# Kernel optimization log

Hardware: AMD Instinct MI355X
Metric: run time of the kernel (lower is better)

## Reference

```python
import jax, jax.numpy as jnp
import numpy as np

N_HIDDEN = 1024
N_OUT = 8
BATCH = 16
SEQ = 2000
TAU = 0.01
TAU_DEPR = 0.2
TAU_FACIL = 1.5
BETA = 50.0
GAIN = 1.0            # self.gain
ACT_GAIN = 8.0        # activation_gain
ACT_THRESH = 0.5      # activation_thresh
DT = 0.001
NOISE_TAU = 0.01
PROB_C = 0.1


def setup_inputs() -> dict:
    key = jax.random.key(0)
    ks = jax.random.split(key, 10)
    I = jax.random.normal(ks[0], (BATCH, SEQ, 1), dtype=jnp.float32)
    h_0 = jax.random.normal(ks[1], (BATCH, N_HIDDEN), dtype=jnp.float32)
    r_0 = jax.random.uniform(ks[2], (BATCH, N_HIDDEN), dtype=jnp.float32)
    u_0 = jax.random.uniform(ks[3], (BATCH, N_HIDDEN), dtype=jnp.float32)
    # parameters, sized/initialized as in __init__
    W_ih = jax.random.normal(ks[4], (N_HIDDEN, 1), dtype=jnp.float32)
    offset_ih = jnp.zeros((N_HIDDEN,), dtype=jnp.float32)
    w_hidden_std = 1.0 / np.sqrt(PROB_C * N_HIDDEN)
    W_hh = jax.random.normal(ks[5], (N_HIDDEN, N_HIDDEN), dtype=jnp.float32) * w_hidden_std
    W_hz = jax.random.normal(ks[6], (N_OUT, N_HIDDEN), dtype=jnp.float32) * (1.0 / np.sqrt(N_HIDDEN))
    offset_hz = jnp.zeros((N_OUT,), dtype=jnp.float32)
    # p_rel ~ N(0.35, 0.15) resampled into (0, 1]; clip is an equivalent in-range stand-in
    p_rel = jnp.clip(jax.random.normal(ks[7], (N_HIDDEN,), dtype=jnp.float32) * 0.15 + 0.35, 0.05, 1.0)
    # sparse recurrent mask with connection prob 0.1
    W_hh_mask = (jax.random.uniform(ks[8], (N_HIDDEN, N_HIDDEN)) < PROB_C).astype(jnp.float32)
    # block-diagonal readout mask: each output reads a disjoint subset of hidden units
    per = N_HIDDEN // N_OUT
    m = np.zeros((N_OUT, N_HIDDEN), dtype=np.float32)
    for i in range(N_OUT):
        m[i, i * per:(i + 1) * per] = 1.0
    W_hz_mask = jnp.asarray(m)
    return {"I": I, "h_0": h_0, "r_0": r_0, "u_0": u_0,
            "W_ih": W_ih, "offset_ih": offset_ih, "W_hh": W_hh,
            "W_hz": W_hz, "offset_hz": offset_hz, "p_rel": p_rel,
            "W_hh_mask": W_hh_mask, "W_hz_mask": W_hz_mask}


def _run(I, h_0, r_0, u_0, W_ih, offset_ih, W_hh, W_hz, offset_hz, p_rel, W_hh_mask, W_hz_mask):
    presyn = 1.0 / p_rel                      # presyn_scaling [H]
    Wm = GAIN * W_hh * W_hh_mask              # masked recurrent weight [H,H]
    Wz = W_hz * W_hz_mask                     # masked readout [O,H]
    ht0 = jax.nn.sigmoid(ACT_GAIN * (h_0 - ACT_THRESH))
    n0 = jnp.zeros_like(h_0)                  # n_0=None, noise_std=0.0 defaults

    def step(carry, I_t):
        h, r, u, ht, n = carry                # all [B,H], ht = transfer(h_{t-1})
        # noise state: dn/dt = -n/noise_tau (noise_std = 0)
        n_new = n - (n / NOISE_TAU) * DT
        # depression / facilitation (use previous-step values, as in torch loop)
        r_new = r + ((1.0 - r) / TAU_DEPR - BETA * u * r * ht) * DT
        u_new = u + ((p_rel - u) / TAU_FACIL + BETA * p_rel * (1.0 - u) * ht) * DT
        # recurrent drive: (r*u*presyn * ht) @ (gain*W_hh*mask)^T, column scaling is presynaptic
        s = ht * r * u * presyn               # [B,H]
        rec = s @ Wm.T                        # [B,H]
        ext = I_t @ W_ih.T + offset_ih + n    # [B,H]
        h_new = h + ((-h + rec + ext) / TAU) * DT
        ht_new = jax.nn.sigmoid(ACT_GAIN * (h_new - ACT_THRESH))
        z = ht_new @ Wz.T + offset_hz         # [B,O]
        return (h_new, r_new, u_new, ht_new, n_new), (n_new, h_new, r_new, u_new, z)

    _, (n_all, h_all, r_all, u_all, z_all) = jax.lax.scan(
        step, (h_0, r_0, u_0, ht0, n0), jnp.swapaxes(I, 0, 1))
    tp = lambda x: jnp.swapaxes(x, 0, 1)      # [S,B,*] -> [B,S,*]
    return tp(n_all), tp(h_all), tp(r_all), tp(u_all), tp(z_all)


def reference(I, h_0, r_0, u_0, W_ih, offset_ih, W_hh, W_hz, offset_hz, p_rel, W_hh_mask, W_hz_mask):
    return _run(I, h_0, r_0, u_0, W_ih, offset_ih, W_hh, W_hz, offset_hz, p_rel, W_hh_mask, W_hz_mask)
```

## Files before the change

kernel.cpp:

```cpp
#include <hip/hip_runtime.h>
#include <cstdint>
#include <cstddef>

typedef float f32x4 __attribute__((ext_vector_type(4)));
typedef unsigned int u32x4 __attribute__((ext_vector_type(4)));
typedef short s16x8 __attribute__((ext_vector_type(8)));

#define H     1024
#define BATCH 16
#define SEQ   2000
#define NOUT  8
#define G     64
#define RPW   16
#define TPB   256

#define H_OFF 32768000
#define R_OFF 65536000
#define U_OFF 98304000
#define Z_OFF 131072000

#define SBUF_OFF  8192
#define IREP_OFF  139264
#define ZPART_OFF 267392

#define TAG(tau) ((unsigned int)(((tau) >> 1) & 1))

__global__ void init_kernel(const float* __restrict__ I, float* __restrict__ Irep,
                            unsigned int* __restrict__ sbuf) {
  int tid = blockIdx.x * blockDim.x + threadIdx.x;
  if (tid < SEQ * BATCH) {
    int t = tid >> 4, b = tid & 15;
    Irep[tid] = I[b * SEQ + t];
  }
  if (tid < 2 * BATCH * H) {
    unsigned int* ap = sbuf + tid; unsigned int v = 1u;
    asm volatile("global_store_dword %0, %1, off sc0 sc1" :: "v"(ap), "v"(v) : "memory");
  }
}

__device__ __forceinline__ unsigned int pack_split(float f) {
  unsigned int uh = __float_as_uint(f) & 0xffff0000u;
  float fl = f - __uint_as_float(uh);
  return uh | (__float_as_uint(fl) >> 16);
}

__global__ __launch_bounds__(TPB, 1) void rnn_persist(
    const float* __restrict__ h0, const float* __restrict__ r0, const float* __restrict__ u0,
    const float* __restrict__ Wih, const float* __restrict__ offih,
    const float* __restrict__ Whh, const float* __restrict__ Whz,
    const float* __restrict__ prel, const float* __restrict__ Whhm, const float* __restrict__ Whzm,
    const float* __restrict__ Irep, unsigned int* __restrict__ sbuf,
    float* __restrict__ zpart, float* __restrict__ dout)
{
  __shared__ float redC[2][4][16][17];

  const int g = blockIdx.x, tid = threadIdx.x;
  const int lane = tid & 63, w = tid >> 6;
  const int arow  = lane & 15;
  const int klane = lane >> 4;
  const int ro = lane >> 2, bo = (w << 2) + (lane & 3);
  const int row = g * RPW + ro;

  s16x8 ahi[8], alo[8];
  {
    const float* wr = Whh  + (size_t)(g * RPW + arow) * H;
    const float* mr = Whhm + (size_t)(g * RPW + arow) * H;
    #pragma unroll
    for (int c = 0; c < 8; ++c) {
      const int jb = w * 256 + c * 32 + klane * 8;
      f32x4 w0 = *(const f32x4*)(wr + jb),     m0 = *(const f32x4*)(mr + jb);
      f32x4 w1 = *(const f32x4*)(wr + jb + 4), m1 = *(const f32x4*)(mr + jb + 4);
      float wf[8] = { w0.x*m0.x, w0.y*m0.y, w0.z*m0.z, w0.w*m0.w,
                      w1.x*m1.x, w1.y*m1.y, w1.z*m1.z, w1.w*m1.w };
      #pragma unroll
      for (int i = 0; i < 8; ++i) {
        unsigned int uh = __float_as_uint(wf[i]) & 0xffff0000u;
        float fl = wf[i] - __uint_as_float(uh);
        ahi[c][i] = (short)(uh >> 16);
        alo[c][i] = (short)(__float_as_uint(fl) >> 16);
      }
    }
  }

  const int sidx = bo * H + row;
  float h  = h0[sidx], rr_ = r0[sidx], u = u0[sidx];
  float p  = prel[row], psyn = 1.0f / p;
  float wih = Wih[row], oih = offih[row];
  float wz = Whz[(row >> 7) * H + row] * Whzm[(row >> 7) * H + row];
  float ht = 1.0f / (1.0f + __expf(-8.0f * (h - 0.5f)));

  const float INV_TAU = 1.0f / 0.01f, INV_TD = 1.0f / 0.2f, INV_TF = 1.0f / 1.5f;
  const int sidx3 = ((row >> 3) << 7) + (bo << 3) + (row & 7);

#define WAITV(n) { asm volatile("s_waitcnt vmcnt(" #n ")" ::: "memory"); \
                   __builtin_amdgcn_sched_barrier(0); }

  {
    unsigned int pk = (pack_split(ht * rr_ * u * psyn) & ~1u) | TAG(0);
    unsigned int* ap = sbuf + sidx3;
    asm volatile("global_store_dword %0, %1, off sc0 sc1" :: "v"(ap), "v"(pk) : "memory");
  }

  float* ph = dout + H_OFF + (size_t)bo * (SEQ * H) + row;
  float* pr = dout + R_OFF + (size_t)bo * (SEQ * H) + row;
  float* pu = dout + U_OFF + (size_t)bo * (SEQ * H) + row;
  float* pz = zpart + (size_t)g * BATCH + (w << 2) + lane;
  const float* ip = Irep + bo;
  float Itc = ip[0];

#define ISSUE_CHUNK(c) { \
    const unsigned int* ap = sb + ((w * 32 + (c) * 4 + klane) * 128 + arow * 8); \
    asm volatile("global_load_dwordx4 %0, %1, off sc0 sc1" : "=v"(ld[2*(c)])   : "v"(ap)     : "memory"); \
    asm volatile("global_load_dwordx4 %0, %1, off sc0 sc1" : "=v"(ld[2*(c)+1]) : "v"(ap + 4) : "memory"); }

#define VCHK(c, okv) { u32x4 v0 = ld[2*(c)], v1 = ld[2*(c)+1]; \
    unsigned int bad = (v0.x ^ tg) | (v0.y ^ tg) | (v0.z ^ tg) | (v0.w ^ tg) \
                     | (v1.x ^ tg) | (v1.y ^ tg) | (v1.z ^ tg) | (v1.w ^ tg); \
    okv = __all((int)((bad & 1u) == 0)); }

#define DO_CHUNK(c) { \
    u32x4 q0 = ld[2*(c)], q1 = ld[2*(c)+1]; \
    s16x8 bh, bl; \
    bh[0]=(short)(q0.x>>16); bl[0]=(short)q0.x; \
    bh[1]=(short)(q0.y>>16); bl[1]=(short)q0.y; \
    bh[2]=(short)(q0.z>>16); bl[2]=(short)q0.z; \
    bh[3]=(short)(q0.w>>16); bl[3]=(short)q0.w; \
    bh[4]=(short)(q1.x>>16); bl[4]=(short)q1.x; \
    bh[5]=(short)(q1.y>>16); bl[5]=(short)q1.y; \
    bh[6]=(short)(q1.z>>16); bl[6]=(short)q1.z; \
    bh[7]=(short)(q1.w>>16); bl[7]=(short)q1.w; \
    acc = __builtin_amdgcn_mfma_f32_16x16x32_bf16(ahi[c], bh, acc, 0, 0, 0); \
    acc = __builtin_amdgcn_mfma_f32_16x16x32_bf16(ahi[c], bl, acc, 0, 0, 0); \
    acc = __builtin_amdgcn_mfma_f32_16x16x32_bf16(alo[c], bh, acc, 0, 0, 0); \
    acc = __builtin_amdgcn_mfma_f32_16x16x32_bf16(alo[c], bl, acc, 0, 0, 0); }

#define FIRST_PASS(c, n) { WAITV(n); int ok; VCHK(c, ok); \
    if (ok) { DO_CHUNK(c); done |= (1 << (c)); } }

  for (int t = 0; t < SEQ; ++t) {
    const unsigned int tg = TAG(t);
    const unsigned int* sb = sbuf + (t & 1) * (BATCH * H);

    u32x4 ld[16];
    f32x4 acc = {0.f, 0.f, 0.f, 0.f};
    int done = 0;

    ISSUE_CHUNK(0) ISSUE_CHUNK(1) ISSUE_CHUNK(2) ISSUE_CHUNK(3)
    ISSUE_CHUNK(4) ISSUE_CHUNK(5) ISSUE_CHUNK(6) ISSUE_CHUNK(7)

    FIRST_PASS(0,14) FIRST_PASS(1,12) FIRST_PASS(2,10) FIRST_PASS(3,8)
    FIRST_PASS(4,6)  FIRST_PASS(5,4)  FIRST_PASS(6,2)  FIRST_PASS(7,0)

    {
      int guard = 0;
      while (done != 0xff && ++guard < (1 << 13)) {
        #pragma unroll
        for (int c = 0; c < 8; ++c)
          if (!(done & (1 << c))) ISSUE_CHUNK(c);
        WAITV(0);
        #pragma unroll
        for (int c = 0; c < 8; ++c)
          if (!(done & (1 << c))) {
            int ok; VCHK(c, ok);
            if (ok) { DO_CHUNK(c); done |= (1 << c); }
          }
      }
    }

    const int pbuf = t & 1;
    redC[pbuf][w][klane * 4 + 0][arow] = acc.x;
    redC[pbuf][w][klane * 4 + 1][arow] = acc.y;
    redC[pbuf][w][klane * 4 + 2][arow] = acc.z;
    redC[pbuf][w][klane * 4 + 3][arow] = acc.w;
    __syncthreads();
    float rec = redC[pbuf][0][ro][bo] + redC[pbuf][1][ro][bo]
              + redC[pbuf][2][ro][bo] + redC[pbuf][3][ro][bo];

    float ext = Itc * wih + oih;
    float hn  = h + ((-h + rec + ext) * INV_TAU) * 0.001f;
    float htn = 1.0f / (1.0f + __expf(-8.0f * (hn - 0.5f)));
    float rn  = rr_ + ((1.0f - rr_) * INV_TD - 50.0f * u * rr_ * ht) * 0.001f;
    float un  = u + ((p - u) * INV_TF + 50.0f * p * (1.0f - u) * ht) * 0.001f;

    {
      unsigned int pk = (pack_split(htn * rn * un * psyn) & ~1u) | TAG(t + 1);
      unsigned int* ap = sbuf + ((t + 1) & 1) * (BATCH * H) + sidx3;
      asm volatile("global_store_dword %0, %1, off sc0 sc1" :: "v"(ap), "v"(pk) : "memory");
    }

    ph[(size_t)t * H] = hn; pr[(size_t)t * H] = rn; pu[(size_t)t * H] = un;
    float zl = htn * wz;
    zl += __shfl_xor(zl, 4); zl += __shfl_xor(zl, 8);
    zl += __shfl_xor(zl, 16); zl += __shfl_xor(zl, 32);
    if (lane < 4) pz[(size_t)t * (G * BATCH)] = zl;

    Itc = ip[(size_t)(t + 1) * BATCH];
    h = hn; ht = htn; rr_ = rn; u = un;
  }
#undef FIRST_PASS
#undef DO_CHUNK
#undef VCHK
#undef ISSUE_CHUNK
#undef WAITV
}

__global__ void zred_kernel(const float* __restrict__ zpart, const float* __restrict__ offhz,
                            float* __restrict__ zout) {
  int tid = blockIdx.x * blockDim.x + threadIdx.x;
  if (tid >= BATCH * SEQ * NOUT) return;
  int b = tid / (SEQ * NOUT);
  int rem = tid - b * (SEQ * NOUT);
  int t = rem >> 3, o = rem & 7;
  float acc = offhz[o];
  #pragma unroll
  for (int k = 0; k < G / NOUT; ++k)
    acc += zpart[((size_t)t * G + o * (G / NOUT) + k) * BATCH + b];
  zout[tid] = acc;
}

extern "C" void kernel_launch(void* const* d_in, const int* in_sizes, int n_in,
                              void* d_out, int out_size, void* d_ws, size_t ws_size,
                              hipStream_t stream) {
  const float* I     = (const float*)d_in[0];
  const float* h0    = (const float*)d_in[1];
  const float* r0    = (const float*)d_in[2];
  const float* u0    = (const float*)d_in[3];
  const float* Wih   = (const float*)d_in[4];
  const float* offih = (const float*)d_in[5];
  const float* Whh   = (const float*)d_in[6];
  const float* Whz   = (const float*)d_in[7];
  const float* offhz = (const float*)d_in[8];
  const float* prel  = (const float*)d_in[9];
  const float* Whhm  = (const float*)d_in[10];
  const float* Whzm  = (const float*)d_in[11];
  float* out = (float*)d_out;

  unsigned int* sbuf  = (unsigned int*)((char*)d_ws + SBUF_OFF);
  float* Irep  = (float*)((char*)d_ws + IREP_OFF);
  float* zpart = (float*)((char*)d_ws + ZPART_OFF);

  hipMemsetAsync(d_out, 0, (size_t)H_OFF * sizeof(float), stream);
  init_kernel<<<128, 256, 0, stream>>>(I, Irep, sbuf);
  rnn_persist<<<G, TPB, 0, stream>>>(h0, r0, u0, Wih, offih, Whh, Whz, prel, Whhm, Whzm,
                                     Irep, sbuf, zpart, out);
  zred_kernel<<<(BATCH * SEQ * NOUT + 255) / 256, 256, 0, stream>>>(zpart, offhz, out + Z_OFF);
}
```

Baseline: 4.616 ms.

## Halve persistent block count by giving each block two 16-row MFMA tiles

Each persistent workgroup now owns 32 hidden rows instead of 16, so the grid shrinks from 64 to 32 blocks. Each wave keeps two sets of split-bf16 weight fragments and issues two MFMA chains per loaded chunk of the broadcast state vector. This halves the number of blocks polling and reading the shared state buffer each step. The per-thread epilogue now handles two rows with vectorized stores, and the readout partial sums are reduced in shared memory and written one step late. The tradeoffs are twice the MFMA work per block on the serial critical path and higher register pressure.

```diff
diff --git a/kernel.cpp b/kernel.cpp
--- a/kernel.cpp
+++ b/kernel.cpp
@@ -3,15 +3,17 @@
 #include <cstddef>
 
 typedef float f32x4 __attribute__((ext_vector_type(4)));
+typedef float f32x2 __attribute__((ext_vector_type(2)));
 typedef unsigned int u32x4 __attribute__((ext_vector_type(4)));
+typedef unsigned int u32x2 __attribute__((ext_vector_type(2)));
 typedef short s16x8 __attribute__((ext_vector_type(8)));
 
 #define H     1024
 #define BATCH 16
 #define SEQ   2000
 #define NOUT  8
-#define G     64
-#define RPW   16
+#define G     32
+#define ROWS  32
 #define TPB   256
 
 #define H_OFF 32768000
@@ -52,59 +54,72 @@
     const float* __restrict__ Irep, unsigned int* __restrict__ sbuf,
     float* __restrict__ zpart, float* __restrict__ dout)
 {
-  __shared__ float redC[2][4][16][17];
+  __shared__ float redC[2][4][2][16][17];
+  __shared__ float zsc[2][4][16];
 
   const int g = blockIdx.x, tid = threadIdx.x;
   const int lane = tid & 63, w = tid >> 6;
   const int arow  = lane & 15;
   const int klane = lane >> 4;
-  const int ro = lane >> 2, bo = (w << 2) + (lane & 3);
-  const int row = g * RPW + ro;
-
-  s16x8 ahi[8], alo[8];
-  {
-    const float* wr = Whh  + (size_t)(g * RPW + arow) * H;
-    const float* mr = Whhm + (size_t)(g * RPW + arow) * H;
+
+  s16x8 ahi[2][8], alo[2][8];
+  #pragma unroll
+  for (int rt = 0; rt < 2; ++rt) {
+    const float* wr = Whh  + (size_t)(g * ROWS + rt * 16 + arow) * H + w * 256 + klane * 8;
+    const float* mr = Whhm + (size_t)(g * ROWS + rt * 16 + arow) * H + w * 256 + klane * 8;
     #pragma unroll
     for (int c = 0; c < 8; ++c) {
-      const int jb = w * 256 + c * 32 + klane * 8;
-      f32x4 w0 = *(const f32x4*)(wr + jb),     m0 = *(const f32x4*)(mr + jb);
-      f32x4 w1 = *(const f32x4*)(wr + jb + 4), m1 = *(const f32x4*)(mr + jb + 4);
+      f32x4 w0 = *(const f32x4*)(wr + c * 32),     m0 = *(const f32x4*)(mr + c * 32);
+      f32x4 w1 = *(const f32x4*)(wr + c * 32 + 4), m1 = *(const f32x4*)(mr + c * 32 + 4);
       float wf[8] = { w0.x*m0.x, w0.y*m0.y, w0.z*m0.z, w0.w*m0.w,
                       w1.x*m1.x, w1.y*m1.y, w1.z*m1.z, w1.w*m1.w };
       #pragma unroll
       for (int i = 0; i < 8; ++i) {
         unsigned int uh = __float_as_uint(wf[i]) & 0xffff0000u;
         float fl = wf[i] - __uint_as_float(uh);
-        ahi[c][i] = (short)(uh >> 16);
-        alo[c][i] = (short)(__float_as_uint(fl) >> 16);
+        ahi[rt][c][i] = (short)(uh >> 16);
+        alo[rt][c][i] = (short)(__float_as_uint(fl) >> 16);
       }
     }
   }
 
-  const int sidx = bo * H + row;
-  float h  = h0[sidx], rr_ = r0[sidx], u = u0[sidx];
-  float p  = prel[row], psyn = 1.0f / p;
-  float wih = Wih[row], oih = offih[row];
-  float wz = Whz[(row >> 7) * H + row] * Whzm[(row >> 7) * H + row];
-  float ht = 1.0f / (1.0f + __expf(-8.0f * (h - 0.5f)));
+  const int r0w = g * ROWS + w * 8 + 2 * klane;
+  const int bo  = arow;
+  f32x2 hv = *(const f32x2*)(h0 + (size_t)bo * H + r0w);
+  f32x2 rv = *(const f32x2*)(r0 + (size_t)bo * H + r0w);
+  f32x2 uv = *(const f32x2*)(u0 + (size_t)bo * H + r0w);
+  f32x2 pv = *(const f32x2*)(prel + r0w);
+  f32x2 wihv = *(const f32x2*)(Wih + r0w);
+  f32x2 oihv = *(const f32x2*)(offih + r0w);
+  const int o = r0w >> 7;
+  f32x2 wzv  = *(const f32x2*)(Whz  + (size_t)o * H + r0w);
+  f32x2 wzm  = *(const f32x2*)(Whzm + (size_t)o * H + r0w);
+  f32x2 psynv, htv;
+  #pragma unroll
+  for (int i = 0; i < 2; ++i) {
+    wzv[i] *= wzm[i];
+    psynv[i] = 1.0f / pv[i];
+    htv[i] = 1.0f / (1.0f + __expf(-8.0f * (hv[i] - 0.5f)));
+  }
 
   const float INV_TAU = 1.0f / 0.01f, INV_TD = 1.0f / 0.2f, INV_TF = 1.0f / 1.5f;
-  const int sidx3 = ((row >> 3) << 7) + (bo << 3) + (row & 7);
+
+  unsigned int* pubp = sbuf + (((r0w >> 3) << 7) + (bo << 3) + (r0w & 7));
 
 #define WAITV(n) { asm volatile("s_waitcnt vmcnt(" #n ")" ::: "memory"); \
                    __builtin_amdgcn_sched_barrier(0); }
 
   {
-    unsigned int pk = (pack_split(ht * rr_ * u * psyn) & ~1u) | TAG(0);
-    unsigned int* ap = sbuf + sidx3;
-    asm volatile("global_store_dword %0, %1, off sc0 sc1" :: "v"(ap), "v"(pk) : "memory");
-  }
-
-  float* ph = dout + H_OFF + (size_t)bo * (SEQ * H) + row;
-  float* pr = dout + R_OFF + (size_t)bo * (SEQ * H) + row;
-  float* pu = dout + U_OFF + (size_t)bo * (SEQ * H) + row;
-  float* pz = zpart + (size_t)g * BATCH + (w << 2) + lane;
+    u32x2 pk;
+    #pragma unroll
+    for (int i = 0; i < 2; ++i)
+      pk[i] = (pack_split(htv[i] * rv[i] * uv[i] * psynv[i]) & ~1u) | TAG(0);
+    asm volatile("global_store_dwordx2 %0, %1, off sc0 sc1" :: "v"(pubp), "v"(pk) : "memory");
+  }
+
+  float* ph = dout + H_OFF + (size_t)bo * (SEQ * H) + r0w;
+  float* pr = dout + R_OFF + (size_t)bo * (SEQ * H) + r0w;
+  float* pu = dout + U_OFF + (size_t)bo * (SEQ * H) + r0w;
   const float* ip = Irep + bo;
   float Itc = ip[0];
 
@@ -129,10 +144,11 @@
     bh[5]=(short)(q1.y>>16); bl[5]=(short)q1.y; \
     bh[6]=(short)(q1.z>>16); bl[6]=(short)q1.z; \
     bh[7]=(short)(q1.w>>16); bl[7]=(short)q1.w; \
-    acc = __builtin_amdgcn_mfma_f32_16x16x32_bf16(ahi[c], bh, acc, 0, 0, 0); \
-    acc = __builtin_amdgcn_mfma_f32_16x16x32_bf16(ahi[c], bl, acc, 0, 0, 0); \
-    acc = __builtin_amdgcn_mfma_f32_16x16x32_bf16(alo[c], bh, acc, 0, 0, 0); \
-    acc = __builtin_amdgcn_mfma_f32_16x16x32_bf16(alo[c], bl, acc, 0, 0, 0); }
+    _Pragma("unroll") for (int rt = 0; rt < 2; ++rt) { \
+      acc[rt] = __builtin_amdgcn_mfma_f32_16x16x32_bf16(ahi[rt][c], bh, acc[rt], 0, 0, 0); \
+      acc[rt] = __builtin_amdgcn_mfma_f32_16x16x32_bf16(ahi[rt][c], bl, acc[rt], 0, 0, 0); \
+      acc[rt] = __builtin_amdgcn_mfma_f32_16x16x32_bf16(alo[rt][c], bh, acc[rt], 0, 0, 0); \
+      acc[rt] = __builtin_amdgcn_mfma_f32_16x16x32_bf16(alo[rt][c], bl, acc[rt], 0, 0, 0); } }
 
 #define FIRST_PASS(c, n) { WAITV(n); int ok; VCHK(c, ok); \
     if (ok) { DO_CHUNK(c); done |= (1 << (c)); } }
@@ -142,7 +158,7 @@
     const unsigned int* sb = sbuf + (t & 1) * (BATCH * H);
 
     u32x4 ld[16];
-    f32x4 acc = {0.f, 0.f, 0.f, 0.f};
+    f32x4 acc[2] = {{0.f,0.f,0.f,0.f},{0.f,0.f,0.f,0.f}};
     int done = 0;
 
     ISSUE_CHUNK(0) ISSUE_CHUNK(1) ISSUE_CHUNK(2) ISSUE_CHUNK(3)
@@ -167,35 +183,61 @@
       }
     }
 
-    const int pbuf = t & 1;
-    redC[pbuf][w][klane * 4 + 0][arow] = acc.x;
-    redC[pbuf][w][klane * 4 + 1][arow] = acc.y;
-    redC[pbuf][w][klane * 4 + 2][arow] = acc.z;
-    redC[pbuf][w][klane * 4 + 3][arow] = acc.w;
+    const int pb = t & 1;
+    #pragma unroll
+    for (int rt = 0; rt < 2; ++rt) {
+      redC[pb][w][rt][klane * 4 + 0][arow] = acc[rt][0];
+      redC[pb][w][rt][klane * 4 + 1][arow] = acc[rt][1];
+      redC[pb][w][rt][klane * 4 + 2][arow] = acc[rt][2];
+      redC[pb][w][rt][klane * 4 + 3][arow] = acc[rt][3];
+    }
     __syncthreads();
-    float rec = redC[pbuf][0][ro][bo] + redC[pbuf][1][ro][bo]
-              + redC[pbuf][2][ro][bo] + redC[pbuf][3][ro][bo];
-
-    float ext = Itc * wih + oih;
-    float hn  = h + ((-h + rec + ext) * INV_TAU) * 0.001f;
-    float htn = 1.0f / (1.0f + __expf(-8.0f * (hn - 0.5f)));
-    float rn  = rr_ + ((1.0f - rr_) * INV_TD - 50.0f * u * rr_ * ht) * 0.001f;
-    float un  = u + ((p - u) * INV_TF + 50.0f * p * (1.0f - u) * ht) * 0.001f;
+
+    if (t > 0 && w == 0 && lane < 16) {
+      const int zp = (t - 1) & 1;
+      float zs = zsc[zp][0][lane] + zsc[zp][1][lane] + zsc[zp][2][lane] + zsc[zp][3][lane];
+      zpart[((size_t)(t - 1) * G + g) * BATCH + lane] = zs;
+    }
+
+    const int rtile = w >> 1, rbase = (w & 1) * 8 + 2 * klane;
+    f32x2 rec;
+    #pragma unroll
+    for (int i = 0; i < 2; ++i)
+      rec[i] = redC[pb][0][rtile][rbase + i][arow] + redC[pb][1][rtile][rbase + i][arow]
+             + redC[pb][2][rtile][rbase + i][arow] + redC[pb][3][rtile][rbase + i][arow];
+
+    f32x2 hn, htn, rn, un; u32x2 pk;
+    #pragma unroll
+    for (int i = 0; i < 2; ++i) {
+      float ext = Itc * wihv[i] + oihv[i];
+      hn[i]  = hv[i] + ((-hv[i] + rec[i] + ext) * INV_TAU) * 0.001f;
+      htn[i] = 1.0f / (1.0f + __expf(-8.0f * (hn[i] - 0.5f)));
+      rn[i]  = rv[i] + ((1.0f - rv[i]) * INV_TD - 50.0f * uv[i] * rv[i] * htv[i]) * 0.001f;
+      un[i]  = uv[i] + ((pv[i] - uv[i]) * INV_TF + 50.0f * pv[i] * (1.0f - uv[i]) * htv[i]) * 0.001f;
+      pk[i]  = (pack_split(htn[i] * rn[i] * un[i] * psynv[i]) & ~1u) | TAG(t + 1);
+    }
 
     {
-      unsigned int pk = (pack_split(htn * rn * un * psyn) & ~1u) | TAG(t + 1);
-      unsigned int* ap = sbuf + ((t + 1) & 1) * (BATCH * H) + sidx3;
-      asm volatile("global_store_dword %0, %1, off sc0 sc1" :: "v"(ap), "v"(pk) : "memory");
-    }
-
-    ph[(size_t)t * H] = hn; pr[(size_t)t * H] = rn; pu[(size_t)t * H] = un;
-    float zl = htn * wz;
-    zl += __shfl_xor(zl, 4); zl += __shfl_xor(zl, 8);
+      unsigned int* ap = pubp + ((t + 1) & 1) * (BATCH * H);
+      asm volatile("global_store_dwordx2 %0, %1, off sc0 sc1" :: "v"(ap), "v"(pk) : "memory");
+    }
+
+    *(f32x2*)(ph + (size_t)t * H) = hn;
+    *(f32x2*)(pr + (size_t)t * H) = rn;
+    *(f32x2*)(pu + (size_t)t * H) = un;
+    float zl = htn[0] * wzv[0] + htn[1] * wzv[1];
     zl += __shfl_xor(zl, 16); zl += __shfl_xor(zl, 32);
-    if (lane < 4) pz[(size_t)t * (G * BATCH)] = zl;
+    if (lane < 16) zsc[t & 1][w][lane] = zl;
 
     Itc = ip[(size_t)(t + 1) * BATCH];
-    h = hn; ht = htn; rr_ = rn; u = un;
+    hv = hn; htv = htn; rv = rn; uv = un;
+  }
+
+  __syncthreads();
+  if (w == 0 && lane < 16) {
+    const int zp = (SEQ - 1) & 1;
+    float zs = zsc[zp][0][lane] + zsc[zp][1][lane] + zsc[zp][2][lane] + zsc[zp][3][lane];
+    zpart[((size_t)(SEQ - 1) * G + g) * BATCH + lane] = zs;
   }
 #undef FIRST_PASS
 #undef DO_CHUNK
@@ -213,8 +255,8 @@
   int t = rem >> 3, o = rem & 7;
   float acc = offhz[o];
   #pragma unroll
-  for (int k = 0; k < G / NOUT; ++k)
-    acc += zpart[((size_t)t * G + o * (G / NOUT) + k) * BATCH + b];
+  for (int k = 0; k < 4; ++k)
+    acc += zpart[((size_t)t * G + o * 4 + k) * BATCH + b];
   zout[tid] = acc;
 }
 
```

Result: slower. 4.965 ms (+7.6%).
